# Kernel optimization log

Measured on AMD Instinct MI355X. Metric: run time of the kernel, lower is better.

The kernel has to match this reference:

```python
import jax, jax.numpy as jnp
import numpy as np

K = 3  # kernel_size
S = 1  # stride
P = 1  # padding


def setup_inputs() -> dict:
    key = jax.random.key(0)
    ks = jax.random.split(key, 5)
    B, C, H, W, O = 4, 64, 128, 128, 64
    x = jax.random.normal(ks[0], (B, C, H, W), jnp.float32)
    # offset conv params (module inits these to 0; use small random values so the
    # bilinear-gather path is actually exercised with non-integer offsets)
    w_off = jax.random.normal(ks[1], (2 * K * K, C, K, K), jnp.float32) * 0.01
    b_off = jax.random.normal(ks[2], (2 * K * K,), jnp.float32) * 0.01
    # deformable conv params (torchvision DeformConv2d has bias=True by default)
    w_dcn = jax.random.normal(ks[3], (O, C, K, K), jnp.float32) * (1.0 / np.sqrt(C * K * K))
    b_dcn = jax.random.normal(ks[4], (O,), jnp.float32) * 0.01
    return {"x": x, "w_off": w_off, "b_off": b_off, "w_dcn": w_dcn, "b_dcn": b_dcn}


def _conv(x, w, b):
    y = jax.lax.conv_general_dilated(
        x, w, window_strides=(S, S), padding=[(P, P), (P, P)],
        dimension_numbers=("NCHW", "OIHW", "NCHW"))
    return y + b[None, :, None, None]


def _deform_conv2d(x, offset, w_dcn, b_dcn):
    # x: [B,C,H,W]; offset: [B, 2*K*K, Ho, Wo] with (dy, dx) interleaved per
    # kernel tap (row-major kh*K+kw), matching torchvision deform_conv2d.
    B, C, H, W = x.shape
    Ho, Wo = offset.shape[2], offset.shape[3]
    K2 = K * K
    off = offset.reshape(B, K2, 2, Ho, Wo)
    oy, ox = off[:, :, 0], off[:, :, 1]  # [B,K2,Ho,Wo]

    kh = (jnp.arange(K2) // K).astype(jnp.float32)
    kw = (jnp.arange(K2) % K).astype(jnp.float32)
    base_y = (jnp.arange(Ho) * S - P).astype(jnp.float32)
    base_x = (jnp.arange(Wo) * S - P).astype(jnp.float32)
    # fractional sampling locations: p0 + p_k + offset
    py = base_y[None, None, :, None] + kh[None, :, None, None] + oy  # [B,K2,Ho,Wo]
    px = base_x[None, None, None, :] + kw[None, :, None, None] + ox

    y0f = jnp.floor(py); x0f = jnp.floor(px)
    dy = py - y0f; dx = px - x0f
    y0 = y0f.astype(jnp.int32); x0 = x0f.astype(jnp.int32)

    def gather(yi, xi):
        # implicit zero padding: mask out-of-range corners
        valid = (yi >= 0) & (yi < H) & (xi >= 0) & (xi < W)
        yc = jnp.clip(yi, 0, H - 1)
        xc = jnp.clip(xi, 0, W - 1)
        v = jax.vmap(lambda xb, yb, xib: xb[:, yb, xib])(x, yc, xc)  # [B,C,K2,Ho,Wo]
        return v * valid[:, None].astype(x.dtype)

    v00 = gather(y0, x0)
    v01 = gather(y0, x0 + 1)
    v10 = gather(y0 + 1, x0)
    v11 = gather(y0 + 1, x0 + 1)

    wy = dy[:, None]; wx = dx[:, None]  # [B,1,K2,Ho,Wo]
    sampled = (v00 * (1 - wy) * (1 - wx) + v01 * (1 - wy) * wx
               + v10 * wy * (1 - wx) + v11 * wy * wx)  # [B,C,K2,Ho,Wo]

    O = w_dcn.shape[0]
    out = jnp.einsum("bckij,ock->boij", sampled, w_dcn.reshape(O, C, K2))
    return out + b_dcn[None, :, None, None]


def reference(x, w_off, b_off, w_dcn, b_dcn):
    offset = _conv(x, w_off, b_off)          # [B, 2*K*K, Ho, Wo]
    return _deform_conv2d(x, offset, w_dcn, b_dcn)
```

## Files before the change

### kernel.cpp

```cpp
#include <hip/hip_runtime.h>
#include <hip/hip_fp16.h>

#define B_ 4
#define H_ 128
#define W_ 128
#define HW_ 16384

typedef _Float16 half8 __attribute__((ext_vector_type(8)));
typedef float floatx16 __attribute__((ext_vector_type(16)));
typedef __attribute__((address_space(3))) void lds_void;
typedef const __attribute__((address_space(1))) void gbl_void;


__global__ __launch_bounds__(256) void k_prep(
    const float* __restrict__ x, const float* __restrict__ w_dcn,
    const float* __restrict__ w_off,
    __half* __restrict__ W2L, __half* __restrict__ W0L,
    _Float16* __restrict__ xh)
{
    int bid = blockIdx.x;
    int t = threadIdx.x;
    if (bid < 2048) {
        int idx = bid*256 + t;
        int p  = idx & (HW_-1);
        int bc = idx >> 14;
        const float* s = x + (size_t)bc*8*HW_ + p;
        half8 vv;
        #pragma unroll
        for (int e = 0; e < 8; ++e) vv[e] = (_Float16)s[e*HW_];
        *(half8*)(xh + (size_t)idx*8) = vv;
    } else {
        int idx = (bid - 2048)*256 + t;
        if (idx < 36864) {
            int e = idx & 7, lane = (idx>>3) & 63, og = (idx>>9) & 1;
            int ks = (idx>>10) & 3, tap = idx >> 12;
            int o = og*32 + (lane & 31);
            int c = ks*16 + (lane >> 5)*8 + e;
            W2L[idx] = __float2half(w_dcn[o*576 + c*9 + tap]);
        } else {
            int i2 = idx - 36864;
            int e = i2 & 7, lane = (i2>>3) & 63;
            int ks = (i2>>9) & 3, tap = i2 >> 11;
            int oc = lane & 31;
            int c = ks*16 + (lane >> 5)*8 + e;
            W0L[i2] = (oc < 18) ? __float2half(w_off[oc*576 + c*9 + tap])
                                : __float2half(0.f);
        }
    }
}

#define CHS2 3456
#define WLOC_OFF 27648
#define SMEM_SZ 36864

__global__ __launch_bounds__(128, 2) void k_fused(
    const _Float16* __restrict__ xh,
    const _Float16* __restrict__ W2L, const _Float16* __restrict__ W0L,
    const float* __restrict__ b_off, const float* __restrict__ b_dcn,
    float* __restrict__ out)
{
    __shared__ __attribute__((aligned(16))) char smem[SMEM_SZ];
    char* halo_c = smem;

    int t = threadIdx.x;
    int lane = t & 63;
    int v = __builtin_amdgcn_readfirstlane(t >> 6);
    int c31 = lane & 31;
    int h8  = lane >> 5;

    char*  wl   = smem + WLOC_OFF + v*4608;
    float* offL = (float*)wl;
    char*  desc = wl;

    int bid  = blockIdx.x;
    int xcd  = bid & 7, sidx = bid >> 3;
    int orig = xcd*128 + sidx;
    int b    = orig >> 8;
    int rem  = orig & 255;
    int i0   = (rem >> 2) * 2;
    int j0   = (rem & 3) * 32;

    {
        int nst  = 14 - v;
        int base = v * 14;
        const _Float16* xhb = xh + ((size_t)b << 20);
        #pragma unroll 1
        for (int s = 0; s < nst; ++s) {
            int i   = base + s;
            int idx = (i << 6) + lane;
            int ch  = idx / 216;
            int pl  = idx - ch*216;
            int hr  = pl / 36;
            int hx  = pl - hr*36;
            int grow = min(max(i0 - 2 + hr, 0), H_-1);
            int gcol = min(max(j0 - 2 + hx, 0), W_-1);
            const _Float16* g = xhb + ((size_t)ch << 17) + (size_t)(((grow<<7) + gcol) << 3);
            __builtin_amdgcn_global_load_lds((gbl_void*)g,
                                             (lds_void*)(halo_c + (i << 10)),
                                             16, 0, 0);
        }
    }
    __syncthreads();

    floatx16 accA = {0.f,0.f,0.f,0.f,0.f,0.f,0.f,0.f,0.f,0.f,0.f,0.f,0.f,0.f,0.f,0.f};
    const half8 hz = {0,0,0,0,0,0,0,0};
    #pragma unroll 1
    for (int tap = 0; tap < 9; ++tap) {
        int kh = tap/3, kw = tap - (tap/3)*3;
        int ii = i0 + v - 1 + kh;
        int jj = j0 + c31 - 1 + kw;
        bool valid = (ii >= 0) && (ii < H_) && (jj >= 0) && (jj < W_);
        int pixA = (v + 1 + kh)*36 + (c31 + 1 + kw);
        #pragma unroll
        for (int s = 0; s < 4; ++s) {
            half8 a = *(const half8*)(halo_c + (s*2 + h8)*CHS2 + pixA*16);
            a = valid ? a : hz;
            half8 bf = *(const half8*)(W0L + ((tap*4+s)<<9) + (lane<<3));
            accA = __builtin_amdgcn_mfma_f32_32x32x16_f16(a, bf, accA, 0, 0, 0);
        }
    }
    {
        int oc = c31;
        if (oc < 18) {
            float bo = b_off[oc];
            #pragma unroll
            for (int r = 0; r < 16; ++r) {
                int row = (r & 3) + 8*(r >> 2) + 4*h8;
                offL[row*18 + oc] = accA[r] + bo;
            }
        }
    }

    float2 o2r[5];
    #pragma unroll
    for (int e = 0; e < 5; ++e) {
        int idx = e*64 + lane;
        if (idx < 288) {
            int pl = idx / 9, tap = idx - pl*9;
            o2r[e] = *(const float2*)(offL + pl*18 + 2*tap);
        }
    }
    uint4 dreg[5];
    #pragma unroll
    for (int e = 0; e < 5; ++e) {
        int idx = e*64 + lane;
        if (idx < 288) {
            int pl = idx / 9, tap = idx - pl*9;
            int kh = tap/3, kw = tap - (tap/3)*3;
            float py = (float)(i0 + v - 1 + kh) + o2r[e].x;
            float px = (float)(j0 + pl - 1 + kw) + o2r[e].y;
            float y0f = floorf(py), x0f = floorf(px);
            float dy = py - y0f, dx = px - x0f;
            int y0 = (int)y0f, x0i = (int)x0f;
            int y1 = y0 + 1,  x1 = x0i + 1;
            bool vy0 = (y0>=0)&(y0<H_),   vy1 = (y1>=0)&(y1<H_);
            bool vx0 = (x0i>=0)&(x0i<W_), vx1 = (x1>=0)&(x1<W_);
            int yc0 = min(max(y0,0),H_-1),  yc1 = min(max(y1,0),H_-1);
            int xc0 = min(max(x0i,0),W_-1), xc1 = min(max(x1,0),W_-1);
            float w00 = (1.f-dy)*(1.f-dx) * ((vy0&&vx0)?1.f:0.f);
            float w01 = (1.f-dy)*dx       * ((vy0&&vx1)?1.f:0.f);
            float w10 = dy*(1.f-dx)       * ((vy1&&vx0)?1.f:0.f);
            float w11 = dy*dx             * ((vy1&&vx1)?1.f:0.f);
            int hy0 = yc0 - (i0-2), hy1 = yc1 - (i0-2);
            int hx0 = xc0 - (j0-2), hx1 = xc1 - (j0-2);
            bool inh = ((unsigned)hy0 < 6u) & ((unsigned)hy1 < 6u)
                     & ((unsigned)hx0 < 36u) & ((unsigned)hx1 < 36u);
            unsigned a0,a1,a2,a3;
            if (inh) { a0 = hy0*36+hx0; a1 = hy0*36+hx1; a2 = hy1*36+hx0; a3 = hy1*36+hx1; }
            else     { a0 = ((yc0<<7)+xc0) | 0x8000u; a1 = (yc0<<7)+xc1;
                       a2 = (yc1<<7)+xc0;             a3 = (yc1<<7)+xc1; }
            __half2 hw0 = __floats2half2_rn(w00, w01);
            __half2 hw1 = __floats2half2_rn(w10, w11);
            dreg[e].x = a0 | (a1 << 16);
            dreg[e].y = a2 | (a3 << 16);
            dreg[e].z = *(unsigned*)&hw0;
            dreg[e].w = *(unsigned*)&hw1;
        }
    }
    #pragma unroll
    for (int e = 0; e < 5; ++e) {
        int idx = e*64 + lane;
        if (idx < 288) {
            int pl = idx / 9, tap = idx - pl*9;
            *(uint4*)(desc + (tap*32 + pl)*16) = dreg[e];
        }
    }

    floatx16 acc0 = {0.f,0.f,0.f,0.f,0.f,0.f,0.f,0.f,0.f,0.f,0.f,0.f,0.f,0.f,0.f,0.f};
    floatx16 acc1 = acc0;

    const char* hqs0 = halo_c + (0*2 + h8)*CHS2;
    const char* hqs1 = halo_c + (1*2 + h8)*CHS2;
    const char* hqs2 = halo_c + (2*2 + h8)*CHS2;
    const char* hqs3 = halo_c + (3*2 + h8)*CHS2;
    const _Float16* xq0 = xh + (((size_t)(b*8) + 0 + h8) << 17);
    const _Float16* xq1 = xh + (((size_t)(b*8) + 2 + h8) << 17);
    const _Float16* xq2 = xh + (((size_t)(b*8) + 4 + h8) << 17);
    const _Float16* xq3 = xh + (((size_t)(b*8) + 6 + h8) << 17);

    #pragma unroll 1
    for (int tap = 0; tap < 9; ++tap) {
        uint4 d = *(const uint4*)(desc + (tap*32 + c31)*16);
        unsigned p0i = d.x & 0x7fffu, p1i = d.x >> 16;
        unsigned p2i = d.y & 0xffffu, p3i = d.y >> 16;
        bool inh = (d.x & 0x8000u) == 0u;
        unsigned short b00 = (unsigned short)(d.z & 0xffffu);
        unsigned short b01 = (unsigned short)(d.z >> 16);
        unsigned short b10 = (unsigned short)(d.w & 0xffffu);
        unsigned short b11 = (unsigned short)(d.w >> 16);
        _Float16 h00 = *(_Float16*)&b00, h01 = *(_Float16*)&b01;
        _Float16 h10 = *(_Float16*)&b10, h11 = *(_Float16*)&b11;
        half8 W00 = {h00,h00,h00,h00,h00,h00,h00,h00};
        half8 W01 = {h01,h01,h01,h01,h01,h01,h01,h01};
        half8 W10 = {h10,h10,h10,h10,h10,h10,h10,h10};
        half8 W11 = {h11,h11,h11,h11,h11,h11,h11,h11};
        half8 sk[4];
        const char* hb[4] = {hqs0, hqs1, hqs2, hqs3};
        const _Float16* xq[4] = {xq0, xq1, xq2, xq3};
        #pragma unroll
        for (int s = 0; s < 4; ++s) {
            half8 v00, v01, v10, v11;
            if (inh) {
                v00 = *(const half8*)(hb[s] + p0i*16);
                v01 = *(const half8*)(hb[s] + p1i*16);
                v10 = *(const half8*)(hb[s] + p2i*16);
                v11 = *(const half8*)(hb[s] + p3i*16);
            } else {
                v00 = *(const half8*)(xq[s] + (size_t)p0i*8);
                v01 = *(const half8*)(xq[s] + (size_t)p1i*8);
                v10 = *(const half8*)(xq[s] + (size_t)p2i*8);
                v11 = *(const half8*)(xq[s] + (size_t)p3i*8);
            }
            sk[s] = v00*W00 + v01*W01 + v10*W10 + v11*W11;
        }
        #pragma unroll
        for (int s = 0; s < 4; ++s) {
            half8 bf0 = *(const half8*)(W2L + (((tap*4+s)*2+0)<<9) + (lane<<3));
            acc0 = __builtin_amdgcn_mfma_f32_32x32x16_f16(sk[s], bf0, acc0, 0, 0, 0);
            half8 bf1 = *(const half8*)(W2L + (((tap*4+s)*2+1)<<9) + (lane<<3));
            acc1 = __builtin_amdgcn_mfma_f32_32x32x16_f16(sk[s], bf1, acc1, 0, 0, 0);
        }
    }
    __syncthreads();

    float* E = (float*)smem;
    #pragma unroll
    for (int r = 0; r < 16; ++r) {
        int row = (r & 3) + 8*(r >> 2) + 4*h8;
        int pl  = v*32 + row;
        E[pl*66 + c31]      = acc0[r];
        E[pl*66 + 32 + c31] = acc1[r];
    }
    __syncthreads();
    int obase = (b*64)*HW_ + i0*W_ + j0;
    int prow = (lane >> 5)*W_ + c31;
    #pragma unroll
    for (int rep = 0; rep < 32; ++rep) {
        int o = rep*2 + v;
        out[obase + o*HW_ + prow] = E[lane*66 + o] + b_dcn[o];
    }
}

extern "C" void kernel_launch(void* const* d_in, const int* in_sizes, int n_in,
                              void* d_out, int out_size, void* d_ws, size_t ws_size,
                              hipStream_t stream) {
    const float* x     = (const float*)d_in[0];
    const float* w_off = (const float*)d_in[1];
    const float* b_off = (const float*)d_in[2];
    const float* w_dcn = (const float*)d_in[3];
    const float* b_dcn = (const float*)d_in[4];
    float* out = (float*)d_out;

    __half* W2L = (__half*)d_ws;
    __half* W0L = (__half*)((char*)d_ws + 73728);
    _Float16* xh = (_Float16*)((char*)d_ws + 110592);

    k_prep<<<2264, 256, 0, stream>>>(x, w_dcn, w_off, W2L, W0L, xh);
    k_fused<<<1024, 128, 0, stream>>>((const _Float16*)xh, (const _Float16*)W2L,
                                      (const _Float16*)W0L, b_off, b_dcn, out);
}
```

Measured before the change: 99.45 us.

## Split offset conv and descriptor build into separate kernel before deformable conv

Moves the offset-conv MFMA and the bilinear descriptor computation out of the fused kernel into a new k_off kernel, which reads directly from global memory and writes per-wave descriptor tables to workspace. The main kernel then loads the halo and the precomputed descriptors into LDS asynchronously in one phase, then runs the gather-MFMA loop. Both tap loops are now partially unrolled. The aim is to shorten the serial critical path of the fused kernel and raise parallelism for the offset stage. The cost is an extra kernel launch and a global round trip for the descriptor tables.

```diff
diff --git a/kernel.cpp b/kernel.cpp
--- a/kernel.cpp
+++ b/kernel.cpp
@@ -49,71 +49,43 @@
     }
 }
 
-#define CHS2 3456
-#define WLOC_OFF 27648
-#define SMEM_SZ 36864
-
-__global__ __launch_bounds__(128, 2) void k_fused(
-    const _Float16* __restrict__ xh,
-    const _Float16* __restrict__ W2L, const _Float16* __restrict__ W0L,
-    const float* __restrict__ b_off, const float* __restrict__ b_dcn,
-    float* __restrict__ out)
+__global__ __launch_bounds__(256, 4) void k_off(
+    const _Float16* __restrict__ xh, const _Float16* __restrict__ W0L,
+    const float* __restrict__ b_off, char* __restrict__ dtab)
 {
-    __shared__ __attribute__((aligned(16))) char smem[SMEM_SZ];
-    char* halo_c = smem;
+    __shared__ __attribute__((aligned(16))) float offLs[4][576];
 
     int t = threadIdx.x;
     int lane = t & 63;
-    int v = __builtin_amdgcn_readfirstlane(t >> 6);
+    int w = __builtin_amdgcn_readfirstlane(t >> 6);
     int c31 = lane & 31;
     int h8  = lane >> 5;
-
-    char*  wl   = smem + WLOC_OFF + v*4608;
-    float* offL = (float*)wl;
-    char*  desc = wl;
-
-    int bid  = blockIdx.x;
-    int xcd  = bid & 7, sidx = bid >> 3;
+    float* offL = offLs[w];
+
+    int T  = blockIdx.x*4 + w;
+    int bt = T >> 1, v = T & 1;
+    int xcd  = bt & 7, sidx = bt >> 3;
     int orig = xcd*128 + sidx;
     int b    = orig >> 8;
     int rem  = orig & 255;
     int i0   = (rem >> 2) * 2;
     int j0   = (rem & 3) * 32;
 
-    {
-        int nst  = 14 - v;
-        int base = v * 14;
-        const _Float16* xhb = xh + ((size_t)b << 20);
-        #pragma unroll 1
-        for (int s = 0; s < nst; ++s) {
-            int i   = base + s;
-            int idx = (i << 6) + lane;
-            int ch  = idx / 216;
-            int pl  = idx - ch*216;
-            int hr  = pl / 36;
-            int hx  = pl - hr*36;
-            int grow = min(max(i0 - 2 + hr, 0), H_-1);
-            int gcol = min(max(j0 - 2 + hx, 0), W_-1);
-            const _Float16* g = xhb + ((size_t)ch << 17) + (size_t)(((grow<<7) + gcol) << 3);
-            __builtin_amdgcn_global_load_lds((gbl_void*)g,
-                                             (lds_void*)(halo_c + (i << 10)),
-                                             16, 0, 0);
-        }
-    }
-    __syncthreads();
-
     floatx16 accA = {0.f,0.f,0.f,0.f,0.f,0.f,0.f,0.f,0.f,0.f,0.f,0.f,0.f,0.f,0.f,0.f};
     const half8 hz = {0,0,0,0,0,0,0,0};
-    #pragma unroll 1
+    #pragma unroll 3
     for (int tap = 0; tap < 9; ++tap) {
         int kh = tap/3, kw = tap - (tap/3)*3;
-        int ii = i0 + v - 1 + kh;
-        int jj = j0 + c31 - 1 + kw;
-        bool valid = (ii >= 0) && (ii < H_) && (jj >= 0) && (jj < W_);
-        int pixA = (v + 1 + kh)*36 + (c31 + 1 + kw);
+        int py = i0 + v - 1 + kh;
+        int px = j0 + c31 - 1 + kw;
+        bool valid = (py >= 0) && (py < H_) && (px >= 0) && (px < W_);
+        int pyc = min(max(py, 0), H_-1);
+        int pxc = min(max(px, 0), W_-1);
+        int pix = (pyc << 7) + pxc;
         #pragma unroll
         for (int s = 0; s < 4; ++s) {
-            half8 a = *(const half8*)(halo_c + (s*2 + h8)*CHS2 + pixA*16);
+            const _Float16* xq = xh + (((size_t)(b*8) + s*2 + h8) << 17);
+            half8 a = *(const half8*)(xq + (size_t)pix*8);
             a = valid ? a : hz;
             half8 bf = *(const half8*)(W0L + ((tap*4+s)<<9) + (lane<<3));
             accA = __builtin_amdgcn_mfma_f32_32x32x16_f16(a, bf, accA, 0, 0, 0);
@@ -140,7 +112,7 @@
             o2r[e] = *(const float2*)(offL + pl*18 + 2*tap);
         }
     }
-    uint4 dreg[5];
+    char* dt = dtab + (size_t)T * 4608;
     #pragma unroll
     for (int e = 0; e < 5; ++e) {
         int idx = e*64 + lane;
@@ -171,20 +143,73 @@
                        a2 = (yc1<<7)+xc0;             a3 = (yc1<<7)+xc1; }
             __half2 hw0 = __floats2half2_rn(w00, w01);
             __half2 hw1 = __floats2half2_rn(w10, w11);
-            dreg[e].x = a0 | (a1 << 16);
-            dreg[e].y = a2 | (a3 << 16);
-            dreg[e].z = *(unsigned*)&hw0;
-            dreg[e].w = *(unsigned*)&hw1;
-        }
-    }
-    #pragma unroll
-    for (int e = 0; e < 5; ++e) {
-        int idx = e*64 + lane;
-        if (idx < 288) {
-            int pl = idx / 9, tap = idx - pl*9;
-            *(uint4*)(desc + (tap*32 + pl)*16) = dreg[e];
-        }
-    }
+            uint4 dr;
+            dr.x = a0 | (a1 << 16);
+            dr.y = a2 | (a3 << 16);
+            dr.z = *(unsigned*)&hw0;
+            dr.w = *(unsigned*)&hw1;
+            *(uint4*)(dt + (size_t)idx*16) = dr;
+        }
+    }
+}
+
+#define CHS2 3456
+#define WLOC_OFF 27648
+#define SMEM_SZ 36864
+
+__global__ __launch_bounds__(128, 2) void k_fused(
+    const _Float16* __restrict__ xh, const char* __restrict__ dtab,
+    const _Float16* __restrict__ W2L, const float* __restrict__ b_dcn,
+    float* __restrict__ out)
+{
+    __shared__ __attribute__((aligned(16))) char smem[SMEM_SZ];
+    char* halo_c = smem;
+
+    int t = threadIdx.x;
+    int lane = t & 63;
+    int v = __builtin_amdgcn_readfirstlane(t >> 6);
+    int c31 = lane & 31;
+    int h8  = lane >> 5;
+
+    char* desc = smem + WLOC_OFF + v*4608;
+
+    int bid  = blockIdx.x;
+    int xcd  = bid & 7, sidx = bid >> 3;
+    int orig = xcd*128 + sidx;
+    int b    = orig >> 8;
+    int rem  = orig & 255;
+    int i0   = (rem >> 2) * 2;
+    int j0   = (rem & 3) * 32;
+
+    {
+        int nst  = 14 - v;
+        int base = v * 14;
+        const _Float16* xhb = xh + ((size_t)b << 20);
+        for (int s = 0; s < nst; ++s) {
+            int i   = base + s;
+            int idx = (i << 6) + lane;
+            int ch  = idx / 216;
+            int pl  = idx - ch*216;
+            int hr  = pl / 36;
+            int hx  = pl - hr*36;
+            int grow = min(max(i0 - 2 + hr, 0), H_-1);
+            int gcol = min(max(j0 - 2 + hx, 0), W_-1);
+            const _Float16* g = xhb + ((size_t)ch << 17) + (size_t)(((grow<<7) + gcol) << 3);
+            __builtin_amdgcn_global_load_lds((gbl_void*)g,
+                                             (lds_void*)(halo_c + (i << 10)),
+                                             16, 0, 0);
+        }
+        const char* dt = dtab + (size_t)(bid*2 + v) * 4608;
+        #pragma unroll
+        for (int i = 0; i < 5; ++i) {
+            int off = i*1024 + lane*16;
+            if (off < 4608)
+                __builtin_amdgcn_global_load_lds((gbl_void*)(dt + off),
+                                                 (lds_void*)(desc + i*1024),
+                                                 16, 0, 0);
+        }
+    }
+    __syncthreads();
 
     floatx16 acc0 = {0.f,0.f,0.f,0.f,0.f,0.f,0.f,0.f,0.f,0.f,0.f,0.f,0.f,0.f,0.f,0.f};
     floatx16 acc1 = acc0;
@@ -198,9 +223,9 @@
     const _Float16* xq2 = xh + (((size_t)(b*8) + 4 + h8) << 17);
     const _Float16* xq3 = xh + (((size_t)(b*8) + 6 + h8) << 17);
 
-    #pragma unroll 1
+    #pragma unroll 3
     for (int tap = 0; tap < 9; ++tap) {
-        uint4 d = *(const uint4*)(desc + (tap*32 + c31)*16);
+        uint4 d = *(const uint4*)(desc + (c31*9 + tap)*16);
         unsigned p0i = d.x & 0x7fffu, p1i = d.x >> 16;
         unsigned p2i = d.y & 0xffffu, p3i = d.y >> 16;
         bool inh = (d.x & 0x8000u) == 0u;
@@ -274,8 +299,11 @@
     __half* W2L = (__half*)d_ws;
     __half* W0L = (__half*)((char*)d_ws + 73728);
     _Float16* xh = (_Float16*)((char*)d_ws + 110592);
+    char* dtab = (char*)d_ws + 8499200;
 
     k_prep<<<2264, 256, 0, stream>>>(x, w_dcn, w_off, W2L, W0L, xh);
-    k_fused<<<1024, 128, 0, stream>>>((const _Float16*)xh, (const _Float16*)W2L,
-                                      (const _Float16*)W0L, b_off, b_dcn, out);
+    k_off<<<512, 256, 0, stream>>>((const _Float16*)xh, (const _Float16*)W0L,
+                                   b_off, dtab);
+    k_fused<<<1024, 128, 0, stream>>>((const _Float16*)xh, dtab,
+                                      (const _Float16*)W2L, b_dcn, out);
 }
```

Measured after the change: 108.7 us. 9.3% more time.
